# Kernel optimization log

Measured on AMD Instinct MI355X. Metric: run time of the kernel, lower is better.

Reference implementation:

```python
import jax, jax.numpy as jnp
import numpy as np


def setup_inputs() -> dict:
    key = jax.random.key(0)
    ks = jax.random.split(key, 5)
    N, D, H, E = 4096, 1024, 4096, 8
    x = jax.random.normal(ks[0], (N, D), dtype=jnp.float32)
    gate_w = jax.random.normal(ks[1], (D, E), dtype=jnp.float32) * (1.0 / np.sqrt(D))
    gate_b = jnp.zeros((E,), dtype=jnp.float32)
    W1 = jax.random.normal(ks[2], (E, D, H), dtype=jnp.float32) * (1.0 / np.sqrt(D))
    b1 = jnp.zeros((E, H), dtype=jnp.float32)
    W2 = jax.random.normal(ks[3], (E, H, D), dtype=jnp.float32) * (1.0 / np.sqrt(H))
    b2 = jnp.zeros((E, D), dtype=jnp.float32)
    return {"x": x, "gate_w": gate_w, "gate_b": gate_b,
            "W1": W1, "b1": b1, "W2": W2, "b2": b2}


def reference(x, gate_w, gate_b, W1, b1, W2, b2):
    # x: [N, D]; W1: [E, D, H]; W2: [E, H, D]
    K = 2
    N, D = x.shape
    E = gate_w.shape[1]
    logits = x @ gate_w + gate_b                      # [N, E]
    probs = jax.nn.softmax(logits, axis=-1)           # [N, E]
    topw, topi = jax.lax.top_k(probs, K)              # [N, K] each; raw probs, not renormalized
    # combine weights as dense [N, E] (zero for unselected experts)
    combine = jnp.zeros((N, E), dtype=x.dtype).at[jnp.arange(N)[:, None], topi].add(topw)
    # batched expert MLP over all experts (dense-dispatch; math identical to top-k combine)
    h = jnp.einsum('nd,edh->enh', x, W1) + b1[:, None, :]   # [E, N, H]
    h = jax.nn.gelu(h, approximate=True)                     # tanh-approx GELU
    y = jnp.einsum('enh,ehd->end', h, W2) + b2[:, None, :]   # [E, N, D]
    out = jnp.einsum('end,ne->nd', y, combine)               # weighted combine
    return out
```

## Files before the change

### kernel.cpp

```cpp
#include <hip/hip_runtime.h>
#include <cstdint>
#include <cstddef>

#define DEVI __device__ __forceinline__

constexpr int N_TOK = 4096, DIM = 1024, HID = 4096, NE = 8;
constexpr int NKR = N_TOK * 2;

typedef __attribute__((ext_vector_type(8))) short short8;
typedef __attribute__((ext_vector_type(4))) float f32x4;

DEVI ushort f2bf(float f) {
  union { float f; uint32_t u; } v; v.f = f;
  uint32_t r = v.u + 0x7FFFu + ((v.u >> 16) & 1u);
  return (ushort)(r >> 16);
}

DEVI float gelu_t(float x) {
  float t = 0.7978845608028654f * (x + 0.044715f * x * x * x);
  t = fminf(fmaxf(t, -15.f), 15.f);
  float e = __expf(2.f * t);
  return 0.5f * x * (1.f + (e - 1.f) / (e + 1.f));
}

DEVI void gload_lds16(const ushort* g, ushort* l) {
  __builtin_amdgcn_global_load_lds(
      (const __attribute__((address_space(1))) void*)g,
      (__attribute__((address_space(3))) void*)l, 16, 0, 0);
}

__global__ void zero_out_kernel(float* __restrict__ out, int n) {
  int i = blockIdx.x * 256 + threadIdx.x;
  if (i < n) out[i] = 0.f;
}

__global__ void convert_x_kernel(const float* __restrict__ x, ushort* __restrict__ xbf) {
  int i = (blockIdx.x * 256 + threadIdx.x) * 4;
  float4 v = *(const float4*)(x + i);
  ushort4 o;
  o.x = f2bf(v.x); o.y = f2bf(v.y); o.z = f2bf(v.z); o.w = f2bf(v.w);
  *(ushort4*)(xbf + i) = o;
}

template<int R, int C>
__global__ void transpose_bf16(const float* __restrict__ src, ushort* __restrict__ dst) {
  __shared__ ushort t[64][68];
  int e = blockIdx.z;
  const float* s = src + (size_t)e * R * C;
  ushort* d = dst + (size_t)e * R * C;
  int r0 = blockIdx.y * 64, c0 = blockIdx.x * 64;
  int lr = threadIdx.x >> 4;
  int lc = (threadIdx.x & 15) * 4;
#pragma unroll
  for (int i = 0; i < 4; ++i) {
    int r = lr + i * 16;
    float4 v = *(const float4*)(s + (size_t)(r0 + r) * C + c0 + lc);
    t[lc + 0][r] = f2bf(v.x);
    t[lc + 1][r] = f2bf(v.y);
    t[lc + 2][r] = f2bf(v.z);
    t[lc + 3][r] = f2bf(v.w);
  }
  __syncthreads();
#pragma unroll
  for (int i = 0; i < 4; ++i) {
    int c = lr + i * 16;
    ushort4 o = *(const ushort4*)&t[c][lc];
    *(ushort4*)(d + (size_t)(c0 + c) * R + r0 + lc) = o;
  }
}

__global__ void gate_kernel(const float* __restrict__ x, const float* __restrict__ gw,
                            const float* __restrict__ gb,
                            int* __restrict__ topi, float* __restrict__ topw,
                            int* __restrict__ counts) {
  int n = blockIdx.x;
  int lane = threadIdx.x;
  double p[NE];
#pragma unroll
  for (int e = 0; e < NE; ++e) p[e] = 0.0;
  const float* xr = x + (size_t)n * DIM;
  for (int d = lane; d < DIM; d += 64) {
    float xv = xr[d];
    const float* g = gw + (size_t)d * NE;
#pragma unroll
    for (int e = 0; e < NE; ++e) p[e] += (double)xv * (double)g[e];
  }
#pragma unroll
  for (int e = 0; e < NE; ++e) {
#pragma unroll
    for (int s = 32; s > 0; s >>= 1) p[e] += __shfl_down(p[e], s);
  }
  if (lane == 0) {
    double m = -1e300;
#pragma unroll
    for (int e = 0; e < NE; ++e) { p[e] += (double)gb[e]; if (p[e] > m) m = p[e]; }
    double s = 0.0, ex[NE];
#pragma unroll
    for (int e = 0; e < NE; ++e) { ex[e] = exp(p[e] - m); s += ex[e]; }
    double inv = 1.0 / s;
    int e0 = 0, e1 = 0; double v0 = -1.0, v1 = -1.0;
#pragma unroll
    for (int e = 0; e < NE; ++e) {
      double pe = ex[e] * inv;
      if (pe > v0)      { v1 = v0; e1 = e0; v0 = pe; e0 = e; }
      else if (pe > v1) { v1 = pe; e1 = e; }
    }
    topi[n * 2] = e0; topi[n * 2 + 1] = e1;
    topw[n * 2] = (float)v0; topw[n * 2 + 1] = (float)v1;
    atomicAdd(&counts[e0], 1);
    atomicAdd(&counts[e1], 1);
  }
}

__global__ void prefix_kernel(const int* __restrict__ counts, int* __restrict__ offs) {
  if (threadIdx.x == 0) {
    int s = 0;
    for (int e = 0; e < NE; ++e) { offs[e] = s; s += counts[e]; }
  }
}

__global__ void scatter_kernel(const int* __restrict__ topi, const float* __restrict__ topw,
                               const int* __restrict__ offs, int* __restrict__ fill,
                               int* __restrict__ tok, float* __restrict__ wgt) {
  int n = blockIdx.x * blockDim.x + threadIdx.x;
  if (n >= N_TOK) return;
#pragma unroll
  for (int k = 0; k < 2; ++k) {
    int e = topi[n * 2 + k];
    int pos = atomicAdd(&fill[e], 1);
    int g = offs[e] + pos;
    tok[g] = n;
    wgt[g] = topw[n * 2 + k];
  }
}

template<int K, bool FIRST>
__global__ __launch_bounds__(256) void moe_gemm(
    const ushort* __restrict__ A,
    const ushort* __restrict__ B,
    const float* __restrict__ bias,
    const int* __restrict__ tok, const float* __restrict__ wgt,
    const int* __restrict__ offs, const int* __restrict__ counts,
    ushort* __restrict__ hbuf, float* __restrict__ out)
{
  constexpr int NCOL = FIRST ? HID : DIM;
  __shared__ ushort Asm[128 * 64];
  __shared__ ushort Bsm[128 * 64];

  const int e = blockIdx.z;
  const int cnt = counts[e];
  const int mbase = blockIdx.y * 128;
  if (mbase >= cnt) return;
  const int off = offs[e];
  const int nbase = blockIdx.x * 128;
  int rv = cnt - mbase; if (rv > 128) rv = 128;

  const int tid = threadIdx.x;
  const int lane = tid & 63, wave = tid >> 6;
  const int sr = tid >> 3;
  const int sc = (tid & 7) * 8;

  const ushort* arow[4];
  const ushort* brow[4];
  const ushort* Be = B + (size_t)e * ((size_t)HID * DIM) + (size_t)nbase * K;
#pragma unroll
  for (int i = 0; i < 4; ++i) {
    int r = sr + 32 * i;
    int rc = r < rv ? r : rv - 1;
    int g = off + mbase + rc;
    long t = FIRST ? (long)tok[g] : (long)g;
    arow[i] = A + t * (long)K + sc;
    brow[i] = Be + (size_t)r * K + sc;
  }

  f32x4 acc[4][4];
#pragma unroll
  for (int a = 0; a < 4; ++a)
#pragma unroll
    for (int b = 0; b < 4; ++b) acc[a][b] = (f32x4)0.f;

  const int quad = lane >> 4, lrow = lane & 15;
  const int wm = (wave >> 1) * 64, wn = (wave & 1) * 64;

  for (int k0 = 0; k0 < K; k0 += 64) {
#pragma unroll
    for (int i = 0; i < 4; ++i) {
      gload_lds16(arow[i] + k0, &Asm[(i * 32 + wave * 8) * 64]);
      gload_lds16(brow[i] + k0, &Bsm[(i * 32 + wave * 8) * 64]);
    }
    __syncthreads();
#pragma unroll
    for (int ks = 0; ks < 2; ++ks) {
      short8 af[4], bf[4];
#pragma unroll
      for (int mt = 0; mt < 4; ++mt)
        af[mt] = *(const short8*)&Asm[(wm + mt * 16 + lrow) * 64 + ks * 32 + quad * 8];
#pragma unroll
      for (int nt = 0; nt < 4; ++nt)
        bf[nt] = *(const short8*)&Bsm[(wn + nt * 16 + lrow) * 64 + ks * 32 + quad * 8];
#pragma unroll
      for (int mt = 0; mt < 4; ++mt)
#pragma unroll
        for (int nt = 0; nt < 4; ++nt)
          acc[mt][nt] = __builtin_amdgcn_mfma_f32_16x16x32_bf16(af[mt], bf[nt], acc[mt][nt], 0, 0, 0);
    }
    __syncthreads();
  }

  if (FIRST) {
#pragma unroll
    for (int mt = 0; mt < 4; ++mt) {
#pragma unroll
      for (int i = 0; i < 4; ++i) {
        int mm = wm + mt * 16 + quad * 4 + i;
        if (mm >= rv) continue;
        size_t g = (size_t)(off + mbase + mm);
#pragma unroll
        for (int nt = 0; nt < 4; ++nt) {
          int col = nbase + wn + nt * 16 + lrow;
          float v = gelu_t(acc[mt][nt][i] + bias[e * NCOL + col]);
          hbuf[g * HID + col] = f2bf(v);
        }
      }
    }
  } else {
#pragma unroll
    for (int mt = 0; mt < 4; ++mt) {
#pragma unroll
      for (int i = 0; i < 4; ++i) {
        int mm = wm + mt * 16 + quad * 4 + i;
        if (mm >= rv) continue;
        int g = off + mbase + mm;
        long t = tok[g];
        float w = wgt[g];
#pragma unroll
        for (int nt = 0; nt < 4; ++nt) {
          int col = nbase + wn + nt * 16 + lrow;
          float v = w * (acc[mt][nt][i] + bias[e * NCOL + col]);
          atomicAdd(out + t * DIM + col, v);
        }
      }
    }
  }
}

extern "C" void kernel_launch(void* const* d_in, const int* in_sizes, int n_in,
                              void* d_out, int out_size, void* d_ws, size_t ws_size,
                              hipStream_t stream) {
  const float* x  = (const float*)d_in[0];
  const float* gw = (const float*)d_in[1];
  const float* gb = (const float*)d_in[2];
  const float* W1 = (const float*)d_in[3];
  const float* b1 = (const float*)d_in[4];
  const float* W2 = (const float*)d_in[5];
  const float* b2 = (const float*)d_in[6];
  float* out = (float*)d_out;

  char* ws = (char*)d_ws;
  size_t o = 0;
  auto alloc = [&](size_t b) { char* p = ws + o; o = (o + b + 255) & ~(size_t)255; return p; };
  int*    tok  = (int*)alloc(NKR * 4);
  float*  wgt  = (float*)alloc(NKR * 4);
  int*    topi = (int*)alloc(N_TOK * 2 * 4);
  float*  topw = (float*)alloc(N_TOK * 2 * 4);
  int*    counts = (int*)alloc(2 * NE * 4);
  int*    fill = counts + NE;
  int*    offs = (int*)alloc(NE * 4);
  ushort* xbf  = (ushort*)alloc((size_t)N_TOK * DIM * 2);
  ushort* hbuf = (ushort*)alloc((size_t)NKR * HID * 2);
  ushort* Wt   = (ushort*)alloc((size_t)NE * HID * DIM * 2);
  size_t need = o;

  zero_out_kernel<<<(out_size + 255) / 256, 256, 0, stream>>>(out, out_size);
  if (ws_size < need) return;

  hipMemsetAsync(counts, 0, 2 * NE * 4, stream);

  convert_x_kernel<<<(N_TOK * DIM / 4) / 256, 256, 0, stream>>>(x, xbf);
  gate_kernel<<<N_TOK, 64, 0, stream>>>(x, gw, gb, topi, topw, counts);
  prefix_kernel<<<1, 64, 0, stream>>>(counts, offs);
  scatter_kernel<<<(N_TOK + 255) / 256, 256, 0, stream>>>(topi, topw, offs, fill, tok, wgt);

  transpose_bf16<DIM, HID><<<dim3(HID / 64, DIM / 64, NE), 256, 0, stream>>>(W1, Wt);
  moe_gemm<DIM, true ><<<dim3(HID / 128, 32, NE), 256, 0, stream>>>(
      xbf, Wt, b1, tok, wgt, offs, counts, hbuf, out);

  transpose_bf16<HID, DIM><<<dim3(DIM / 64, HID / 64, NE), 256, 0, stream>>>(W2, Wt);
  moe_gemm<HID, false><<<dim3(DIM / 128, 32, NE), 256, 0, stream>>>(
      hbuf, Wt, b2, tok, wgt, offs, counts, hbuf, out);
}
```

Measured before the change: 824.2 us.

## Double-buffer MoE GEMM LDS tiles and swizzle workgroup order across XCDs

The MoE GEMM now keeps two LDS buffers and issues the global-to-LDS loads for the next K tile before computing on the current one. It waits with a partial vmcnt so memory latency overlaps the MFMA work. The grid is flattened to 1D and block ids are remapped so consecutive ids on the same XCD cover neighbouring tiles, aiming for better L2 reuse. This doubles LDS use per block, which may lower occupancy, and correctness depends on the hand-set vmcnt(8) matching the eight loads issued per stage.

```diff
diff --git a/kernel.cpp b/kernel.cpp
--- a/kernel.cpp
+++ b/kernel.cpp
@@ -134,7 +134,7 @@
   }
 }
 
-template<int K, bool FIRST>
+template<int K, int NX, bool FIRST>
 __global__ __launch_bounds__(256) void moe_gemm(
     const ushort* __restrict__ A,
     const ushort* __restrict__ B,
@@ -144,15 +144,23 @@
     ushort* __restrict__ hbuf, float* __restrict__ out)
 {
   constexpr int NCOL = FIRST ? HID : DIM;
-  __shared__ ushort Asm[128 * 64];
-  __shared__ ushort Bsm[128 * 64];
-
-  const int e = blockIdx.z;
+  constexpr int TSZ = 128 * 64;
+  __shared__ ushort Asm[2 * TSZ];
+  __shared__ ushort Bsm[2 * TSZ];
+
+  const int nwg = NX * 32 * NE;
+  const int bid = blockIdx.x;
+  const int swz = (bid & 7) * (nwg >> 3) + (bid >> 3);
+  const int e = swz / (NX * 32);
+  const int rem = swz - e * (NX * 32);
+  const int xt = rem >> 5;
+  const int yt = rem & 31;
+
   const int cnt = counts[e];
-  const int mbase = blockIdx.y * 128;
+  const int mbase = yt * 128;
   if (mbase >= cnt) return;
   const int off = offs[e];
-  const int nbase = blockIdx.x * 128;
+  const int nbase = xt * 128;
   int rv = cnt - mbase; if (rv > 128) rv = 128;
 
   const int tid = threadIdx.x;
@@ -182,30 +190,46 @@
   const int quad = lane >> 4, lrow = lane & 15;
   const int wm = (wave >> 1) * 64, wn = (wave & 1) * 64;
 
-  for (int k0 = 0; k0 < K; k0 += 64) {
+  auto stage = [&](int buf, int k0) {
 #pragma unroll
     for (int i = 0; i < 4; ++i) {
-      gload_lds16(arow[i] + k0, &Asm[(i * 32 + wave * 8) * 64]);
-      gload_lds16(brow[i] + k0, &Bsm[(i * 32 + wave * 8) * 64]);
-    }
-    __syncthreads();
+      gload_lds16(arow[i] + k0, &Asm[buf * TSZ + (i * 32 + wave * 8) * 64]);
+      gload_lds16(brow[i] + k0, &Bsm[buf * TSZ + (i * 32 + wave * 8) * 64]);
+    }
+  };
+  auto compute = [&](int buf) {
 #pragma unroll
     for (int ks = 0; ks < 2; ++ks) {
       short8 af[4], bf[4];
 #pragma unroll
       for (int mt = 0; mt < 4; ++mt)
-        af[mt] = *(const short8*)&Asm[(wm + mt * 16 + lrow) * 64 + ks * 32 + quad * 8];
+        af[mt] = *(const short8*)&Asm[buf * TSZ + (wm + mt * 16 + lrow) * 64 + ks * 32 + quad * 8];
 #pragma unroll
       for (int nt = 0; nt < 4; ++nt)
-        bf[nt] = *(const short8*)&Bsm[(wn + nt * 16 + lrow) * 64 + ks * 32 + quad * 8];
+        bf[nt] = *(const short8*)&Bsm[buf * TSZ + (wn + nt * 16 + lrow) * 64 + ks * 32 + quad * 8];
 #pragma unroll
       for (int mt = 0; mt < 4; ++mt)
 #pragma unroll
         for (int nt = 0; nt < 4; ++nt)
           acc[mt][nt] = __builtin_amdgcn_mfma_f32_16x16x32_bf16(af[mt], bf[nt], acc[mt][nt], 0, 0, 0);
     }
-    __syncthreads();
-  }
+  };
+
+  constexpr int NK = K / 64;
+  stage(0, 0);
+  int cur = 0;
+  for (int t = 0; t + 1 < NK; ++t) {
+    stage(cur ^ 1, (t + 1) * 64);
+    asm volatile("s_waitcnt vmcnt(8)" ::: "memory");
+    __builtin_amdgcn_s_barrier();
+    __builtin_amdgcn_sched_barrier(0);
+    compute(cur);
+    __builtin_amdgcn_sched_barrier(0);
+    __builtin_amdgcn_s_barrier();
+    cur ^= 1;
+  }
+  __syncthreads();
+  compute(cur);
 
   if (FIRST) {
 #pragma unroll
@@ -282,10 +306,10 @@
   scatter_kernel<<<(N_TOK + 255) / 256, 256, 0, stream>>>(topi, topw, offs, fill, tok, wgt);
 
   transpose_bf16<DIM, HID><<<dim3(HID / 64, DIM / 64, NE), 256, 0, stream>>>(W1, Wt);
-  moe_gemm<DIM, true ><<<dim3(HID / 128, 32, NE), 256, 0, stream>>>(
+  moe_gemm<DIM, HID / 128, true ><<<dim3((HID / 128) * 32 * NE), 256, 0, stream>>>(
       xbf, Wt, b1, tok, wgt, offs, counts, hbuf, out);
 
   transpose_bf16<HID, DIM><<<dim3(DIM / 64, HID / 64, NE), 256, 0, stream>>>(W2, Wt);
-  moe_gemm<HID, false><<<dim3(DIM / 128, 32, NE), 256, 0, stream>>>(
+  moe_gemm<HID, DIM / 128, false><<<dim3((DIM / 128) * 32 * NE), 256, 0, stream>>>(
       hbuf, Wt, b2, tok, wgt, offs, counts, hbuf, out);
 }
```

Measured after the change: 880.9 us. 6.9% more time.
